# Performance work log

Measured on AMD Instinct MI355X. Metric: run time of the kernel, lower is better.

The kernel has to match this reference:

```python
import jax, jax.numpy as jnp
import numpy as np

EPS = 1e-5

def _conv(x, w, pad):
    return jax.lax.conv_general_dilated(
        x, w, (1, 1), [(pad, pad), (pad, pad)],
        dimension_numbers=('NCHW', 'OIHW', 'NCHW'))

def _bn(x, gamma, beta):
    # BatchNorm2d in training mode: batch statistics over (B,H,W)
    m = jnp.mean(x, axis=(0, 2, 3), keepdims=True)
    v = jnp.var(x, axis=(0, 2, 3), keepdims=True)
    return gamma.reshape(1, -1, 1, 1) * (x - m) * jax.lax.rsqrt(v + EPS) + beta.reshape(1, -1, 1, 1)

def setup_inputs() -> dict:
    key = jax.random.key(0)
    ks = jax.random.split(key, 8)
    B, C, H, W = 2, 128, 128, 128
    E, G, K = 32, 3, 3
    k2 = K * K
    s = 0.05
    return {
        'feat': jax.random.normal(ks[0], (B, C, H, W), jnp.float32),
        'guide': jax.random.normal(ks[1], (B, G, 2 * H, 2 * W), jnp.float32),
        'g_w1': jax.random.normal(ks[2], (E, G, 3, 3), jnp.float32) * s,
        'g_g1': jnp.ones((E,), jnp.float32),
        'g_b1': jnp.zeros((E,), jnp.float32),
        'g_w2': jax.random.normal(ks[3], (E, E, 3, 3), jnp.float32) * s,
        'g_g2': jnp.ones((E,), jnp.float32),
        'g_b2': jnp.zeros((E,), jnp.float32),
        'p_w': jax.random.normal(ks[4], (E, C, 1, 1), jnp.float32) * s,
        'k_w1': jax.random.normal(ks[5], (E, 2 * E, 3, 3), jnp.float32) * s,
        'k_w2': jax.random.normal(ks[6], (k2, E, 1, 1), jnp.float32) * s,
        'k_b2': jnp.zeros((k2,), jnp.float32),
    }

def reference(feat, guide, g_w1, g_g1, g_b1, g_w2, g_g2, g_b2, p_w, k_w1, k_w2, k_b2):
    K = 3
    pad = K // 2
    k2 = K * K
    B, C, H, W = feat.shape
    H2, W2 = 2 * H, 2 * W
    feat_up = jnp.repeat(jnp.repeat(feat, 2, axis=2), 2, axis=3)  # (B,C,H2,W2)
    # guide encoder: conv-BN-ReLU x2
    g = jax.nn.relu(_bn(_conv(guide, g_w1, 1), g_g1, g_b1))
    g = jax.nn.relu(_bn(_conv(g, g_w2, 1), g_g2, g_b2))
    # feature projection: 1x1 conv + ReLU
    f = jax.nn.relu(_conv(feat_up, p_w, 0))
    comb = jnp.concatenate([g, f], axis=1)  # (B,2E,H2,W2)
    kern = _conv(jax.nn.relu(_conv(comb, k_w1, 1)), k_w2, 0) + k_b2.reshape(1, -1, 1, 1)
    kern = jax.nn.softmax(kern, axis=1)  # (B,k2,H2,W2)
    # CARAFE-style reassembly without materializing the unfold tensor:
    # out[b,c,y,x] = sum_{dy,dx} kern[b,dy*K+dx,y,x] * feat_up_pad[b,c,y+dy,x+dx]
    fp = jnp.pad(feat_up, ((0, 0), (0, 0), (pad, pad), (pad, pad)))
    out = jnp.zeros((B, C, H2, W2), feat.dtype)
    for i in range(k2):  # fixed small k2=9 taps
        dy, dx = i // K, i % K
        out = out + kern[:, i:i + 1] * fp[:, :, dy:dy + H2, dx:dx + W2]
    return out
```

## Files before the change

kernel.cpp:

```cpp
#include <hip/hip_runtime.h>
#include <hip/hip_bf16.h>

#define EPS 1e-5f


typedef unsigned short ushort_t;
typedef __attribute__((ext_vector_type(8))) short short8v;
typedef __attribute__((ext_vector_type(4))) float f32x4;

__device__ __forceinline__ int swz(int b) { return b ^ (((b >> 7) & 7) << 4); }
__device__ __forceinline__ float bf2f(ushort_t u) {
    unsigned int t = ((unsigned int)u) << 16;
    return __builtin_bit_cast(float, t);
}
__device__ __forceinline__ ushort_t f2bf(float f) {
    __hip_bfloat16 h = (__hip_bfloat16)f;
    return __builtin_bit_cast(ushort_t, h);
}

__device__ __forceinline__ void ab_inline(
    const float* __restrict__ part, const float* __restrict__ gamma,
    const float* __restrict__ beta, float* red, int tid)
{
    int col = tid & 63, quart = tid >> 6;
    float s = 0.f;
    const float* p = part + (size_t)(quart * 128) * 64 + col;
#pragma unroll 8
    for (int bq = 0; bq < 128; ++bq) s += p[(size_t)bq * 64];
    red[quart * 64 + col] = s;
    __syncthreads();
    if (tid < 64)
        red[256 + tid] = red[tid] + red[64 + tid] + red[128 + tid] + red[192 + tid];
    __syncthreads();
    if (tid < 32) {
        float S  = red[256 + (tid >> 1) * 4 + (tid & 1) * 2];
        float SS = red[256 + (tid >> 1) * 4 + (tid & 1) * 2 + 1];
        const float n = 131072.f;
        float mean = S / n;
        float var = SS / n - mean * mean;
        float a = gamma[tid] * rsqrtf(var + EPS);
        red[320 + tid] = a;
        red[352 + tid] = beta[tid] - mean * a;
    }
    __syncthreads();
}

__global__ __launch_bounds__(256) void k_phase1(
    const float* __restrict__ guide, const float* __restrict__ w1,
    const float* __restrict__ w2, const float* __restrict__ kw1,
    const float* __restrict__ pw, const float* __restrict__ feat,
    ushort_t* __restrict__ x1, ushort_t* __restrict__ fs,
    ushort_t* __restrict__ wpk, float* __restrict__ part1)
{
    __shared__ __align__(16) char lds[40960];
    int tid = threadIdx.x;
    int blk = blockIdx.x;

    if (blk < 512) {
        float* smu = (float*)lds;
        int b = blk >> 8;
        int tile = blk & 255;
        int ty0 = (tile >> 4) << 4, tx0 = (tile & 15) << 4;

        for (int i = tid; i < 972; i += 256) {
            int c = i / 324;
            int rem = i - c * 324;
            int r = rem / 18, cl = rem - r * 18;
            int yy = ty0 + r - 1, xx = tx0 + cl - 1;
            float v = 0.f;
            if (yy >= 0 && yy < 256 && xx >= 0 && xx < 256)
                v = guide[((b * 3 + c) * 256 + yy) * 256 + xx];
            smu[c * 342 + r * 19 + cl] = v;
        }
        __syncthreads();

        int r = tid >> 4, cl = tid & 15;
        float t[27];
#pragma unroll
        for (int c = 0; c < 3; ++c)
#pragma unroll
            for (int ky = 0; ky < 3; ++ky)
#pragma unroll
                for (int kx = 0; kx < 3; ++kx)
                    t[c * 9 + ky * 3 + kx] = smu[c * 342 + (r + ky) * 19 + cl + kx];
        int y = ty0 + r, x = tx0 + cl;
        float* sdump = (float*)(lds + 4224);
        ushort_t pk[32];
#pragma unroll 4
        for (int e = 0; e < 32; ++e) {
            float acc = 0.f;
#pragma unroll
            for (int k = 0; k < 27; ++k)
                acc += t[k] * w1[e * 27 + k];
            pk[e] = f2bf(acc);
            sdump[tid * 33 + e] = bf2f(pk[e]);
        }
        ushort_t* dst = x1 + ((size_t)(b * 65536 + y * 256 + x)) * 32;
#pragma unroll
        for (int h = 0; h < 4; ++h)
            *(uint4*)(dst + h * 8) = *(uint4*)(pk + h * 8);

        __syncthreads();
        {
            int ch = tid & 31, seg = tid >> 5;
            float s = 0.f, q = 0.f;
#pragma unroll 8
            for (int i = 0; i < 32; ++i) {
                float v = sdump[(seg * 32 + i) * 33 + ch];
                s += v; q += v * v;
            }
            float* segbuf = (float*)(lds + 38016);
            segbuf[(seg * 32 + ch) * 2 + 0] = s;
            segbuf[(seg * 32 + ch) * 2 + 1] = q;
            __syncthreads();
            if (tid < 64) {
                int c = tid >> 1, isq = tid & 1;
                float tt = 0.f;
#pragma unroll
                for (int g = 0; g < 8; ++g)
                    tt += segbuf[(g * 32 + c) * 2 + isq];
                int col = (c >> 1) * 4 + (c & 1) * 2 + isq;
                part1[(size_t)blk * 64 + col] = tt;
            }
        }
    } else if (blk < 768) {
        int row = blk - 512;
        int b = row >> 7, yl = row & 127;
        ushort_t* pwl = (ushort_t*)(lds + 32768);

        for (int i = tid; i < 4096; i += 256) {
            int j = i & 7, l = (i >> 3) & 63, nt = (i >> 9) & 1, ks = i >> 10;
            int e = nt * 16 + (l & 15);
            int c = ks * 32 + (l >> 4) * 8 + j;
            pwl[i] = f2bf(pw[e * 128 + c]);
        }
        int x = tid & 127, cg = tid >> 7;
        const float* fb = feat + ((size_t)b << 21) + yl * 128 + x;
#pragma unroll
        for (int p = 0; p < 8; ++p) {
            int c0 = p * 16 + cg * 8;
            ushort_t pk[8];
#pragma unroll
            for (int j = 0; j < 8; ++j)
                pk[j] = f2bf(fb[(size_t)(c0 + j) << 14]);
            *(uint4*)(lds + swz(x * 256 + c0 * 2)) = *(uint4*)pk;
        }
        __syncthreads();

        int w = tid >> 6, l = tid & 63, lm = l & 15, lg = l >> 4;
        int px0 = w * 32;
        f32x4 acc[2][2] = {};
        const short8v* gB = (const short8v*)pwl;
#pragma unroll
        for (int ks = 0; ks < 4; ++ks) {
            short8v B0 = gB[(ks * 2 + 0) * 64 + l];
            short8v B1 = gB[(ks * 2 + 1) * 64 + l];
#pragma unroll
            for (int m = 0; m < 2; ++m) {
                short8v A = *(const short8v*)(
                    lds + swz((px0 + m * 16 + lm) * 256 + ks * 64 + lg * 16));
                acc[m][0] = __builtin_amdgcn_mfma_f32_16x16x32_bf16(A, B0, acc[m][0], 0, 0, 0);
                acc[m][1] = __builtin_amdgcn_mfma_f32_16x16x32_bf16(A, B1, acc[m][1], 0, 0, 0);
            }
        }
        __syncthreads();
#pragma unroll
        for (int m = 0; m < 2; ++m)
#pragma unroll
            for (int nt = 0; nt < 2; ++nt)
#pragma unroll
                for (int rg = 0; rg < 4; ++rg) {
                    int px = px0 + m * 16 + lg * 4 + rg;
                    int e = nt * 16 + lm;
                    *(ushort_t*)(lds + swz(px * 64 + e * 2)) =
                        f2bf(fmaxf(acc[m][nt][rg], 0.f));
                }
        __syncthreads();
        if (tid < 128) {
            ushort_t* dst = fs + ((size_t)(b * 16384 + yl * 128 + tid)) * 32;
#pragma unroll
            for (int h = 0; h < 4; ++h)
                *(uint4*)(dst + h * 8) = *(uint4*)(lds + swz(tid * 64 + h * 16));
        }
    } else {
        int i = (blk - 768) * 256 + tid;
        if (i < 9216) {
            int j = i & 7, l = (i >> 3) & 63, nt = (i >> 9) & 1, t = i >> 10;
            int e = nt * 16 + (l & 15);
            int k = (l >> 4) * 8 + j;
            wpk[i] = f2bf(w2[(e * 32 + k) * 9 + t]);
        } else {
            int i2 = i - 9216;
            int j = i2 & 7, l = (i2 >> 3) & 63, nt = (i2 >> 9) & 1;
            int kk = (i2 >> 10) & 1, t = i2 >> 11;
            int e = nt * 16 + (l & 15);
            int k = kk * 32 + (l >> 4) * 8 + j;
            wpk[i] = f2bf(kw1[(e * 64 + k) * 9 + t]);
        }
    }
}

__global__ __launch_bounds__(256) void k_conv2(
    const ushort_t* __restrict__ x1, const float* __restrict__ part1,
    const float* __restrict__ gamma, const float* __restrict__ beta,
    const ushort_t* __restrict__ w2pk, ushort_t* __restrict__ x2,
    float* __restrict__ part2)
{
    __shared__ __align__(16) char lds[22784];
    float* red = (float*)(lds + 20736);
    int tid = threadIdx.x;
    ab_inline(part1, gamma, beta, red, tid);
    const float* ab1 = red + 320;

    int b = blockIdx.x >> 8, tile = blockIdx.x & 255;
    int ty0 = (tile >> 4) << 4, tx0 = (tile & 15) << 4;

    for (int i = tid; i < 1296; i += 256) {
        int px = i >> 2, c8 = i & 3;
        int r = px / 18, cl = px - r * 18;
        int yy = ty0 + r - 1, xx = tx0 + cl - 1;
        ushort_t pk[8];
        if (yy >= 0 && yy < 256 && xx >= 0 && xx < 256) {
            const ushort_t* src = x1 + ((size_t)(b * 65536 + yy * 256 + xx)) * 32 + c8 * 8;
            uint4 raw = *(const uint4*)src;
            const ushort_t* rs = (const ushort_t*)&raw;
#pragma unroll
            for (int j = 0; j < 8; ++j) {
                int c = c8 * 8 + j;
                pk[j] = f2bf(fmaxf(ab1[c] * bf2f(rs[j]) + ab1[32 + c], 0.f));
            }
        } else {
#pragma unroll
            for (int j = 0; j < 8; ++j) pk[j] = 0;
        }
        *(uint4*)(lds + swz(px * 64 + c8 * 16)) = *(uint4*)pk;
    }
    __syncthreads();

    int w = tid >> 6, l = tid & 63, lm = l & 15, lg = l >> 4;
    f32x4 acc[4][2] = {};
    const short8v* gB = (const short8v*)w2pk;
#pragma unroll
    for (int t = 0; t < 9; ++t) {
        int ky = t / 3, kx = t % 3;
        short8v B0 = gB[(t * 2 + 0) * 64 + l];
        short8v B1 = gB[(t * 2 + 1) * 64 + l];
#pragma unroll
        for (int m = 0; m < 4; ++m) {
            int px = (w * 4 + m + ky) * 18 + lm + kx;
            short8v A = *(const short8v*)(lds + swz(px * 64 + lg * 16));
            acc[m][0] = __builtin_amdgcn_mfma_f32_16x16x32_bf16(A, B0, acc[m][0], 0, 0, 0);
            acc[m][1] = __builtin_amdgcn_mfma_f32_16x16x32_bf16(A, B1, acc[m][1], 0, 0, 0);
        }
    }
    __syncthreads();
#pragma unroll
    for (int m = 0; m < 4; ++m)
#pragma unroll
        for (int nt = 0; nt < 2; ++nt)
#pragma unroll
            for (int rg = 0; rg < 4; ++rg) {
                int px = (w * 4 + m) * 16 + lg * 4 + rg;
                int e = nt * 16 + lm;
                *(ushort_t*)(lds + swz(px * 64 + e * 2)) = f2bf(acc[m][nt][rg]);
            }
    __syncthreads();
    {
        int px = tid, r = px >> 4, cl = px & 15;
        int yy = ty0 + r, xx = tx0 + cl;
        ushort_t* dst = x2 + ((size_t)(b * 65536 + yy * 256 + xx)) * 32;
#pragma unroll
        for (int h = 0; h < 4; ++h)
            *(uint4*)(dst + h * 8) = *(uint4*)(lds + swz(px * 64 + h * 16));
    }

    {
        int ch = tid & 31, seg = tid >> 5;
        float s = 0.f, q = 0.f;
#pragma unroll 8
        for (int i = 0; i < 32; ++i) {
            int px = seg * 32 + i;
            float v = bf2f(*(const ushort_t*)(lds + swz(px * 64 + ch * 2)));
            s += v; q += v * v;
        }
        float* segbuf = (float*)(lds + 20736);
        __syncthreads();
        segbuf[(seg * 32 + ch) * 2 + 0] = s;
        segbuf[(seg * 32 + ch) * 2 + 1] = q;
        __syncthreads();
        if (tid < 64) {
            int c = tid >> 1, isq = tid & 1;
            float tt = 0.f;
#pragma unroll
            for (int g = 0; g < 8; ++g)
                tt += segbuf[(g * 32 + c) * 2 + isq];
            int col = (c >> 1) * 4 + (c & 1) * 2 + isq;
            part2[(size_t)blockIdx.x * 64 + col] = tt;
        }
    }
}

__global__ __launch_bounds__(256) void k_tail(
    const ushort_t* __restrict__ x2, const float* __restrict__ part2,
    const float* __restrict__ gamma, const float* __restrict__ beta,
    const ushort_t* __restrict__ fs, const ushort_t* __restrict__ kw1pk,
    const float* __restrict__ kw2, const float* __restrict__ kb2,
    const float* __restrict__ feat, float* __restrict__ out)
{
    __shared__ __align__(16) char lds[38784];
    int tid = threadIdx.x;

    int p = blockIdx.x;
    int xcd = p & 7, q = p >> 3;
    int g = xcd * 64 + (q >> 1);
    int b = g >> 8;
    int rem = g & 255;
    int ty0 = (rem >> 3) << 3;
    int tx0 = (((rem & 7) << 1) | (q & 1)) << 4;

    float* redz = (float*)(lds + 32640);
    ab_inline(part2, gamma, beta, redz, tid);
    const float* ab2 = redz + 320;

    for (int i = tid; i < 1440; i += 256) {
        int px = i >> 3, c8 = i & 7;
        int r = px / 18, cl = px - r * 18;
        int yy = ty0 + r - 1, xx = tx0 + cl - 1;
        ushort_t pk[8];
        if (yy >= 0 && yy < 256 && xx >= 0 && xx < 256) {
            if (c8 < 4) {
                const ushort_t* src = x2 + ((size_t)(b * 65536 + yy * 256 + xx)) * 32 + c8 * 8;
                uint4 raw = *(const uint4*)src;
                const ushort_t* rs = (const ushort_t*)&raw;
#pragma unroll
                for (int j = 0; j < 8; ++j) {
                    int c = c8 * 8 + j;
                    pk[j] = f2bf(fmaxf(ab2[c] * bf2f(rs[j]) + ab2[32 + c], 0.f));
                }
            } else {
                const ushort_t* src = fs + ((size_t)(b * 16384 + (yy >> 1) * 128 + (xx >> 1))) * 32 + (c8 - 4) * 8;
                *(uint4*)pk = *(const uint4*)src;
            }
        } else {
#pragma unroll
            for (int j = 0; j < 8; ++j) pk[j] = 0;
        }
        *(uint4*)(lds + swz(px * 128 + c8 * 16)) = *(uint4*)pk;
    }
    __syncthreads();

    int w = tid >> 6, l = tid & 63, lm = l & 15, lg = l >> 4;
    f32x4 acc[2][2] = {};
    {
        const short8v* gB = (const short8v*)kw1pk;
#pragma unroll
        for (int t = 0; t < 9; ++t) {
            int ky = t / 3, kx = t % 3;
#pragma unroll
            for (int kk = 0; kk < 2; ++kk) {
                short8v B0 = gB[(t * 4 + kk * 2 + 0) * 64 + l];
                short8v B1 = gB[(t * 4 + kk * 2 + 1) * 64 + l];
#pragma unroll
                for (int m = 0; m < 2; ++m) {
                    int mt = w * 2 + m;
                    int px = (mt + ky) * 18 + lm + kx;
                    short8v A = *(const short8v*)(lds + swz(px * 128 + kk * 64 + lg * 16));
                    acc[m][0] = __builtin_amdgcn_mfma_f32_16x16x32_bf16(A, B0, acc[m][0], 0, 0, 0);
                    acc[m][1] = __builtin_amdgcn_mfma_f32_16x16x32_bf16(A, B1, acc[m][1], 0, 0, 0);
                }
            }
        }
    }
    __syncthreads();
#pragma unroll
    for (int m = 0; m < 2; ++m)
#pragma unroll
        for (int nt = 0; nt < 2; ++nt)
#pragma unroll
            for (int rg = 0; rg < 4; ++rg) {
                int px = (w * 2 + m) * 16 + lg * 4 + rg;
                int e = nt * 16 + lm;
                *(float*)(lds + swz(px * 128 + e * 4)) = acc[m][nt][rg];
            }
    __syncthreads();

    float* zbuf = (float*)(lds + 32640);
    if (tid < 128) {
        int px = tid;
        float v[32];
#pragma unroll
        for (int h = 0; h < 8; ++h) {
            float4 qd = *(const float4*)(lds + swz(px * 128 + h * 16));
            v[h * 4 + 0] = qd.x; v[h * 4 + 1] = qd.y; v[h * 4 + 2] = qd.z; v[h * 4 + 3] = qd.w;
        }
        float z[9];
#pragma unroll
        for (int i = 0; i < 9; ++i) z[i] = kb2[i];
#pragma unroll
        for (int e = 0; e < 32; ++e) {
            float ae = fmaxf(v[e], 0.f);
#pragma unroll
            for (int i = 0; i < 9; ++i)
                z[i] += ae * kw2[i * 32 + e];
        }
        float m = z[0];
#pragma unroll
        for (int i = 1; i < 9; ++i) m = fmaxf(m, z[i]);
        float sum = 0.f;
#pragma unroll
        for (int i = 0; i < 9; ++i) { z[i] = expf(z[i] - m); sum += z[i]; }
        float inv = 1.f / sum;
#pragma unroll
        for (int i = 0; i < 9; ++i) zbuf[px * 12 + i] = z[i] * inv;
    }
    __syncthreads();

    float* lf2 = (float*)lds;
    {
        int ty0l = ty0 >> 1, tx0l = tx0 >> 1;
        for (int i = tid; i < 3072; i += 256) {
            int c = i / 24;
            int rem2 = i - c * 24;
            int rt = rem2 >> 2, qq = rem2 & 3;
            int ylo = ty0l + rt - 1;
            int cb = tx0l - 4 + qq * 4;
            float4 v = { 0.f, 0.f, 0.f, 0.f };
            if (ylo >= 0 && ylo < 128 && cb >= 0 && cb < 125)
                v = *(const float4*)(feat + (((size_t)(b * 128 + c)) << 14) + ylo * 128 + cb);
            const float* vp = (const float*)&v;
#pragma unroll
            for (int j = 0; j < 4; ++j) {
                int k = cb + j - (tx0l - 1);
                if (k >= 0 && k < 10)
                    lf2[(rt * 10 + k) * 136 + c] = vp[j];
            }
        }
    }
    __syncthreads();

    {
        int px = tid & 127, chalf = tid >> 7;
        int r = px >> 4, cl = px & 15;
        int y = ty0 + r, x = tx0 + cl;
        int ry = r & 1, rx = cl & 1;
        float z[9];
#pragma unroll
        for (int i = 0; i < 9; ++i) z[i] = zbuf[px * 12 + i];
        float zr[2][3];
#pragma unroll
        for (int dx = 0; dx < 3; ++dx) {
            if (ry == 0) { zr[0][dx] = z[dx];             zr[1][dx] = z[3 + dx] + z[6 + dx]; }
            else         { zr[0][dx] = z[dx] + z[3 + dx]; zr[1][dx] = z[6 + dx]; }
        }
        float co00, co01, co10, co11;
        if (rx == 0) { co00 = zr[0][0];            co01 = zr[0][1] + zr[0][2];
                       co10 = zr[1][0];            co11 = zr[1][1] + zr[1][2]; }
        else         { co00 = zr[0][0] + zr[0][1]; co01 = zr[0][2];
                       co10 = zr[1][0] + zr[1][1]; co11 = zr[1][2]; }
        int py0 = (r >> 1) + ry, px0c = (cl >> 1) + rx;
        int p00 = py0 * 10 + px0c;
        float* op = out + (((size_t)b * 128) * 256 + y) * 256 + x;
#pragma unroll 4
        for (int gg = 0; gg < 16; ++gg) {
            int c4 = chalf * 16 + gg;
            float4 f00 = *(const float4*)(lf2 + p00 * 136 + c4 * 4);
            float4 f01 = *(const float4*)(lf2 + (p00 + 1) * 136 + c4 * 4);
            float4 f10 = *(const float4*)(lf2 + (p00 + 10) * 136 + c4 * 4);
            float4 f11 = *(const float4*)(lf2 + (p00 + 11) * 136 + c4 * 4);
            const float* a00 = (const float*)&f00;
            const float* a01 = (const float*)&f01;
            const float* a10 = (const float*)&f10;
            const float* a11 = (const float*)&f11;
#pragma unroll
            for (int j = 0; j < 4; ++j) {
                float o = co00 * a00[j] + co01 * a01[j]
                        + co10 * a10[j] + co11 * a11[j];
                op[(size_t)(c4 * 4 + j) * 65536] = o;
            }
        }
    }
}

extern "C" void kernel_launch(void* const* d_in, const int* in_sizes, int n_in,
                              void* d_out, int out_size, void* d_ws, size_t ws_size,
                              hipStream_t stream)
{
    const float* feat  = (const float*)d_in[0];
    const float* guide = (const float*)d_in[1];
    const float* g_w1  = (const float*)d_in[2];
    const float* g_g1  = (const float*)d_in[3];
    const float* g_b1  = (const float*)d_in[4];
    const float* g_w2  = (const float*)d_in[5];
    const float* g_g2  = (const float*)d_in[6];
    const float* g_b2  = (const float*)d_in[7];
    const float* p_w   = (const float*)d_in[8];
    const float* k_w1  = (const float*)d_in[9];
    const float* k_w2  = (const float*)d_in[10];
    const float* k_b2  = (const float*)d_in[11];

    float* out = (float*)d_out;

    ushort_t* x1 = (ushort_t*)out;
    ushort_t* x2 = (ushort_t*)(out + 2097152);

    ushort_t* fs    = (ushort_t*)d_ws;
    ushort_t* wpk   = (ushort_t*)((char*)d_ws + 2097152);
    float*    partA = (float*)((char*)d_ws + 2152448);
    float*    partB = (float*)((char*)d_ws + 2283520);
    ushort_t* w2pk  = wpk;
    ushort_t* kw1pk = wpk + 9216;

    k_phase1<<<876, 256, 0, stream>>>(guide, g_w1, g_w2, k_w1, p_w, feat,
                                      x1, fs, wpk, partA);
    k_conv2<<<512, 256, 0, stream>>>(x1, partA, g_g1, g_b1, w2pk, x2, partB);
    k_tail<<<1024, 256, 0, stream>>>(x2, partB, g_g2, g_b2, fs, kw1pk,
                                     k_w2, k_b2, feat, out);
}
```

Measured before the change: 71.47 us.

## Prefetch tail inputs before BN reduction and pair-pixel reassembly with float2 stores

Global loads of the x2 and fs tiles are issued before the inline BN-stat reduction, so their latency overlaps it; the BN/ReLU transform is applied afterwards from registers. Collapsed reassembly coefficients are now computed once in the softmax stage and stored as float4 per pixel. In the reassembly loop each thread handles two adjacent output pixels, sharing the feature reads, and writes float2 stores. The LDS row stride changes from 136 to 140 floats to alter bank mapping. In exchange the prefetch holds more registers.

```diff
diff --git a/kernel.cpp b/kernel.cpp
--- a/kernel.cpp
+++ b/kernel.cpp
@@ -307,7 +307,7 @@
     const float* __restrict__ kw2, const float* __restrict__ kb2,
     const float* __restrict__ feat, float* __restrict__ out)
 {
-    __shared__ __align__(16) char lds[38784];
+    __shared__ __align__(16) char lds[35648];
     int tid = threadIdx.x;
 
     int p = blockIdx.x;
@@ -318,34 +318,47 @@
     int ty0 = (rem >> 3) << 3;
     int tx0 = (((rem & 7) << 1) | (q & 1)) << 4;
 
-    float* redz = (float*)(lds + 32640);
+    for (int i = tid; i < 720; i += 256) {
+        int px = i >> 2, c4 = i & 3;
+        int r = px / 18, cl = px - r * 18;
+        int yy = ty0 + r - 1, xx = tx0 + cl - 1;
+        uint4 v = { 0, 0, 0, 0 };
+        if (yy >= 0 && yy < 256 && xx >= 0 && xx < 256)
+            v = *(const uint4*)(fs + ((size_t)(b * 16384 + (yy >> 1) * 128 + (xx >> 1))) * 32 + c4 * 8);
+        *(uint4*)(lds + swz(px * 128 + (c4 + 4) * 16)) = v;
+    }
+    uint4 raw[3]; bool val[3]; int offs[3];
+#pragma unroll
+    for (int s = 0; s < 3; ++s) {
+        int i = tid + s * 256;
+        int px = i >> 2, c4 = i & 3;
+        int r = px / 18, cl = px - r * 18;
+        int yy = ty0 + r - 1, xx = tx0 + cl - 1;
+        bool inb = (i < 720) && yy >= 0 && yy < 256 && xx >= 0 && xx < 256;
+        val[s] = inb;
+        offs[s] = swz(px * 128 + c4 * 16);
+        uint4 v = { 0, 0, 0, 0 };
+        if (inb)
+            v = *(const uint4*)(x2 + ((size_t)(b * 65536 + yy * 256 + xx)) * 32 + c4 * 8);
+        raw[s] = v;
+        if (i < 720 && !inb) *(uint4*)(lds + offs[s]) = v;
+    }
+
+    float* redz = (float*)(lds + 33600);
     ab_inline(part2, gamma, beta, redz, tid);
     const float* ab2 = redz + 320;
 
-    for (int i = tid; i < 1440; i += 256) {
-        int px = i >> 3, c8 = i & 7;
-        int r = px / 18, cl = px - r * 18;
-        int yy = ty0 + r - 1, xx = tx0 + cl - 1;
-        ushort_t pk[8];
-        if (yy >= 0 && yy < 256 && xx >= 0 && xx < 256) {
-            if (c8 < 4) {
-                const ushort_t* src = x2 + ((size_t)(b * 65536 + yy * 256 + xx)) * 32 + c8 * 8;
-                uint4 raw = *(const uint4*)src;
-                const ushort_t* rs = (const ushort_t*)&raw;
-#pragma unroll
-                for (int j = 0; j < 8; ++j) {
-                    int c = c8 * 8 + j;
-                    pk[j] = f2bf(fmaxf(ab2[c] * bf2f(rs[j]) + ab2[32 + c], 0.f));
-                }
-            } else {
-                const ushort_t* src = fs + ((size_t)(b * 16384 + (yy >> 1) * 128 + (xx >> 1))) * 32 + (c8 - 4) * 8;
-                *(uint4*)pk = *(const uint4*)src;
-            }
-        } else {
-#pragma unroll
-            for (int j = 0; j < 8; ++j) pk[j] = 0;
-        }
-        *(uint4*)(lds + swz(px * 128 + c8 * 16)) = *(uint4*)pk;
+#pragma unroll
+    for (int s = 0; s < 3; ++s) {
+        if (val[s]) {
+            int c0 = ((tid + s * 256) & 3) * 8;
+            const ushort_t* rs = (const ushort_t*)&raw[s];
+            ushort_t pk[8];
+#pragma unroll
+            for (int j = 0; j < 8; ++j)
+                pk[j] = f2bf(fmaxf(ab2[c0 + j] * bf2f(rs[j]) + ab2[32 + c0 + j], 0.f));
+            *(uint4*)(lds + offs[s]) = *(uint4*)pk;
+        }
     }
     __syncthreads();
 
@@ -384,7 +397,7 @@
             }
     __syncthreads();
 
-    float* zbuf = (float*)(lds + 32640);
+    float* coef = (float*)(lds + 33600);
     if (tid < 128) {
         int px = tid;
         float v[32];
@@ -411,7 +424,21 @@
         for (int i = 0; i < 9; ++i) { z[i] = expf(z[i] - m); sum += z[i]; }
         float inv = 1.f / sum;
 #pragma unroll
-        for (int i = 0; i < 9; ++i) zbuf[px * 12 + i] = z[i] * inv;
+        for (int i = 0; i < 9; ++i) z[i] *= inv;
+        int r = px >> 4, cl = px & 15;
+        int ry = r & 1, rx = cl & 1;
+        float zr0[3], zr1[3];
+#pragma unroll
+        for (int dx = 0; dx < 3; ++dx) {
+            if (ry == 0) { zr0[dx] = z[dx];            zr1[dx] = z[3 + dx] + z[6 + dx]; }
+            else         { zr0[dx] = z[dx] + z[3 + dx]; zr1[dx] = z[6 + dx]; }
+        }
+        float4 cf;
+        if (rx == 0) { cf.x = zr0[0];           cf.y = zr0[1] + zr0[2];
+                       cf.z = zr1[0];           cf.w = zr1[1] + zr1[2]; }
+        else         { cf.x = zr0[0] + zr0[1];  cf.y = zr0[2];
+                       cf.z = zr1[0] + zr1[1];  cf.w = zr1[2]; }
+        *(float4*)(coef + px * 4) = cf;
     }
     __syncthreads();
 
@@ -432,50 +459,46 @@
             for (int j = 0; j < 4; ++j) {
                 int k = cb + j - (tx0l - 1);
                 if (k >= 0 && k < 10)
-                    lf2[(rt * 10 + k) * 136 + c] = vp[j];
+                    lf2[(rt * 10 + k) * 140 + c] = vp[j];
             }
         }
     }
     __syncthreads();
 
     {
-        int px = tid & 127, chalf = tid >> 7;
-        int r = px >> 4, cl = px & 15;
-        int y = ty0 + r, x = tx0 + cl;
-        int ry = r & 1, rx = cl & 1;
-        float z[9];
-#pragma unroll
-        for (int i = 0; i < 9; ++i) z[i] = zbuf[px * 12 + i];
-        float zr[2][3];
-#pragma unroll
-        for (int dx = 0; dx < 3; ++dx) {
-            if (ry == 0) { zr[0][dx] = z[dx];             zr[1][dx] = z[3 + dx] + z[6 + dx]; }
-            else         { zr[0][dx] = z[dx] + z[3 + dx]; zr[1][dx] = z[6 + dx]; }
-        }
-        float co00, co01, co10, co11;
-        if (rx == 0) { co00 = zr[0][0];            co01 = zr[0][1] + zr[0][2];
-                       co10 = zr[1][0];            co11 = zr[1][1] + zr[1][2]; }
-        else         { co00 = zr[0][0] + zr[0][1]; co01 = zr[0][2];
-                       co10 = zr[1][0] + zr[1][1]; co11 = zr[1][2]; }
-        int py0 = (r >> 1) + ry, px0c = (cl >> 1) + rx;
-        int p00 = py0 * 10 + px0c;
-        float* op = out + (((size_t)b * 128) * 256 + y) * 256 + x;
-#pragma unroll 4
-        for (int gg = 0; gg < 16; ++gg) {
-            int c4 = chalf * 16 + gg;
-            float4 f00 = *(const float4*)(lf2 + p00 * 136 + c4 * 4);
-            float4 f01 = *(const float4*)(lf2 + (p00 + 1) * 136 + c4 * 4);
-            float4 f10 = *(const float4*)(lf2 + (p00 + 10) * 136 + c4 * 4);
-            float4 f11 = *(const float4*)(lf2 + (p00 + 11) * 136 + c4 * 4);
+        int cq = tid >> 6;
+        int r  = (tid >> 3) & 7;
+        int xp = tid & 7;
+        int y = ty0 + r;
+        int x0 = tx0 + 2 * xp;
+        int pxA = r * 16 + 2 * xp;
+        const float4 cA = *(const float4*)(coef + pxA * 4);
+        const float4 cB = *(const float4*)(coef + pxA * 4 + 4);
+        int py0 = (r >> 1) + (r & 1);
+        int base0 = (py0 * 10 + xp) * 140;
+        int base1 = base0 + 1400;
+        float* op = out + (((size_t)b * 128) * 256 + y) * 256 + x0;
+#pragma unroll 2
+        for (int g8 = 0; g8 < 8; ++g8) {
+            int cb = (cq * 8 + g8) * 4;
+            float4 f00 = *(const float4*)(lf2 + base0 + cb);
+            float4 f01 = *(const float4*)(lf2 + base0 + 140 + cb);
+            float4 f02 = *(const float4*)(lf2 + base0 + 280 + cb);
+            float4 f10 = *(const float4*)(lf2 + base1 + cb);
+            float4 f11 = *(const float4*)(lf2 + base1 + 140 + cb);
+            float4 f12 = *(const float4*)(lf2 + base1 + 280 + cb);
             const float* a00 = (const float*)&f00;
             const float* a01 = (const float*)&f01;
+            const float* a02 = (const float*)&f02;
             const float* a10 = (const float*)&f10;
             const float* a11 = (const float*)&f11;
+            const float* a12 = (const float*)&f12;
 #pragma unroll
             for (int j = 0; j < 4; ++j) {
-                float o = co00 * a00[j] + co01 * a01[j]
-                        + co10 * a10[j] + co11 * a11[j];
-                op[(size_t)(c4 * 4 + j) * 65536] = o;
+                float2 o;
+                o.x = cA.x * a00[j] + cA.y * a01[j] + cA.z * a10[j] + cA.w * a11[j];
+                o.y = cB.x * a01[j] + cB.y * a02[j] + cB.z * a11[j] + cB.w * a12[j];
+                *(float2*)(op + (size_t)(cb + j) * 65536) = o;
             }
         }
     }
```

New measurement: 75.59 us. +5.8%, slower.
